# Kernel optimization log

Hardware: AMD Instinct MI355X
Metric: run time of the kernel (lower is better)

## Reference

```python
import jax, jax.numpy as jnp
import numpy as np

N, E, IN, H, O, K = 50000, 800000, 256, 128, 32, 5
ALPHA, EPS = 0.1, 1e-5


def setup_inputs() -> dict:
    key = jax.random.key(0)
    ks = jax.random.split(key, 20)
    nrm = lambda k, shape, s=0.02: jax.random.normal(k, shape, dtype=jnp.float32) * s
    H2 = H // 2
    return {
        "x": jax.random.normal(ks[0], (N, IN), dtype=jnp.float32),
        "edge_index": jax.random.randint(ks[1], (2, E), 0, N),
        "edge_weight": jax.random.uniform(ks[2], (E,), dtype=jnp.float32),
        # lin1 + bn1
        "W1": nrm(ks[3], (IN, H)), "b1": jnp.zeros((H,), jnp.float32),
        "g1": jnp.ones((H,), jnp.float32), "be1": jnp.zeros((H,), jnp.float32),
        "m1": nrm(ks[4], (H,), 0.1), "v1": 1.0 + 0.1 * jax.random.uniform(ks[5], (H,), dtype=jnp.float32),
        # lin2 + bn2
        "W2": nrm(ks[6], (H, H)), "b2": jnp.zeros((H,), jnp.float32),
        "g2": jnp.ones((H,), jnp.float32), "be2": jnp.zeros((H,), jnp.float32),
        "m2": nrm(ks[7], (H,), 0.1), "v2": 1.0 + 0.1 * jax.random.uniform(ks[8], (H,), dtype=jnp.float32),
        # attention over hop outputs (K+1)
        "att": jnp.ones((K + 1,), jnp.float32) + nrm(ks[9], (K + 1,), 0.1),
        # head: Linear(H, H//2) + BN + ReLU + Linear(H//2, O)
        "W3": nrm(ks[10], (H, H2)), "b3": jnp.zeros((H2,), jnp.float32),
        "g3": jnp.ones((H2,), jnp.float32), "be3": jnp.zeros((H2,), jnp.float32),
        "m3": nrm(ks[11], (H2,), 0.1), "v3": 1.0 + 0.1 * jax.random.uniform(ks[12], (H2,), dtype=jnp.float32),
        "W4": nrm(ks[13], (H2, O)), "b4": jnp.zeros((O,), jnp.float32),
    }


def _bn(t, g, b, m, v):
    # eval-mode BatchNorm1d using running stats
    return (t - m) * (g / jnp.sqrt(v + EPS)) + b


def reference(x, edge_index, edge_weight, W1, b1, g1, be1, m1, v1,
              W2, b2, g2, be2, m2, v2, att,
              W3, b3, g3, be3, m3, v3, W4, b4):
    n = x.shape[0]
    row, col = edge_index[0], edge_index[1]

    h = jax.nn.relu(_bn(x @ W1 + b1, g1, be1, m1, v1))
    identity = h
    h = jax.nn.relu(_bn(h @ W2 + b2, g2, be2, m2, v2)) + identity

    # weighted edge normalization: out-weight sum per source node, clamped >= 1
    wsum = jnp.maximum(jax.ops.segment_sum(edge_weight, row, num_segments=n), 1.0)
    edge_norm = edge_weight / wsum[row]  # [E]

    def prop(h_in):
        # APPNP-style: K inner iterations blending toward this call's h0
        h0 = h_in
        hk = h_in
        for _ in range(K):
            msg = hk[row] * edge_norm[:, None]          # [E, H] gather + scale
            agg = jax.ops.segment_sum(msg, col, num_segments=n)  # scatter-add
            hk = (1.0 - ALPHA) * agg + ALPHA * h0
        return hk

    xs = [h]
    hc = h
    for _ in range(K):  # outer loop: att has K+1 weights
        hc = prop(hc)
        xs.append(hc)

    stacked = jnp.stack(xs, axis=-1)          # [N, H, K+1]
    w = jax.nn.softmax(att)                   # [K+1]
    fused = jnp.einsum('nhk,k->nh', stacked, w)

    hid = jax.nn.relu(_bn(fused @ W3 + b3, g3, be3, m3, v3))
    return hid @ W4 + b4
```

## Files before the change

kernel.cpp:

```cpp
#include <hip/hip_runtime.h>
#include <cstddef>
#include <cstdint>

namespace {

constexpr int N   = 50000;
constexpr int E   = 800000;
constexpr int IN  = 256;
constexpr int H   = 128;
constexpr int H2v = 64;
constexpr int O   = 32;
constexpr int K   = 5;
constexpr float ALPHA = 0.1f;
constexpr float EPS   = 1e-5f;
constexpr int NPAD = 50048;
constexpr int CAP  = 48;
constexpr int NPW  = 4;
constexpr int PROP_BLOCKS = NPAD / (4 * NPW);
constexpr int NORM_BLOCKS = NPAD / 4;
constexpr int MLP_BLOCKS  = NPAD / 64;

typedef __bf16 bf16x8 __attribute__((ext_vector_type(8)));
typedef float  f32x4  __attribute__((ext_vector_type(4)));

__device__ inline uint32_t pack2_bf16(float x, float y) {
  uint32_t ux = __float_as_uint(x);
  uint32_t uy = __float_as_uint(y);
  ux = (ux + 0x7FFFu + ((ux >> 16) & 1u)) >> 16;
  uy = (uy + 0x7FFFu + ((uy >> 16) & 1u)) & 0xFFFF0000u;
  return uy | ux;
}
__device__ inline unsigned short bf16_1(float x) {
  uint32_t u = __float_as_uint(x);
  return (unsigned short)((u + 0x7FFFu + ((u >> 16) & 1u)) >> 16);
}
__device__ inline float bf16_lo(uint32_t v) { return __uint_as_float(v << 16); }
__device__ inline float bf16_hi(uint32_t v) { return __uint_as_float(v & 0xFFFF0000u); }
__device__ inline float bf16_f(unsigned short h) { return __uint_as_float(((uint32_t)h) << 16); }

__global__ void init_kernel(int* __restrict__ cnt, float* __restrict__ wsum,
                            const float* __restrict__ att, float* __restrict__ wk) {
  int i = blockIdx.x * blockDim.x + threadIdx.x;
  if (i < NPAD) cnt[i] = 0;
  if (i < N) wsum[i] = 0.f;
  if (i == 0) {
    float mx = att[0];
    for (int j = 1; j < K + 1; ++j) mx = fmaxf(mx, att[j]);
    float ex[K + 1];
    float s = 0.f;
    for (int j = 0; j < K + 1; ++j) { ex[j] = expf(att[j] - mx); s += ex[j]; }
    for (int j = 0; j < K + 1; ++j) wk[j] = ex[j] / s;
  }
}

__global__ void fused_fill_kernel(const int* __restrict__ row, const int* __restrict__ col,
                                  const float* __restrict__ ew,
                                  int* __restrict__ cnt, float* __restrict__ wsum,
                                  uint2* __restrict__ csr) {
  int i = blockIdx.x * blockDim.x + threadIdx.x;
  if (i < E) {
    int s = row[i];
    float w = ew[i];
    atomicAdd(&wsum[s], w);
    int d = col[i];
    int old = atomicAdd(&cnt[d], 1);
    if (old < CAP) csr[(size_t)d * CAP + old] = make_uint2((uint32_t)s, __float_as_uint(w));
  }
}

__global__ void conv_wt_kernel(const float* __restrict__ W, unsigned short* __restrict__ Wt,
                               int Kdim) {
  int t = blockIdx.x * blockDim.x + threadIdx.x;
  int k8 = Kdim / 8;
  int n = t / k8;
  int kk = (t % k8) * 8;
  if (n >= H) return;
  float f[8];
#pragma unroll
  for (int j = 0; j < 8; ++j) f[j] = W[(size_t)(kk + j) * H + n];
  uint4 pk;
  pk.x = pack2_bf16(f[0], f[1]);
  pk.y = pack2_bf16(f[2], f[3]);
  pk.z = pack2_bf16(f[4], f[5]);
  pk.w = pack2_bf16(f[6], f[7]);
  *(uint4*)&Wt[(size_t)n * Kdim + kk] = pk;
}

__global__ __launch_bounds__(256) void mlp1_mfma_kernel(
    const float* __restrict__ x, const unsigned short* __restrict__ Wt1,
    const float* __restrict__ b1, const float* __restrict__ g1,
    const float* __restrict__ be1, const float* __restrict__ m1,
    const float* __restrict__ v1, unsigned short* __restrict__ h1bf) {
  int wave = threadIdx.x >> 6;
  int lane = threadIdx.x & 63;
  int m_base = blockIdx.x * 64 + wave * 16;
  int idx16 = lane & 15;
  int quad = lane >> 4;
  int m = m_base + idx16;
  bf16x8 afrag[8];
  if (m < N) {
    const float* xrow = x + (size_t)m * IN + quad * 8;
#pragma unroll
    for (int k0 = 0; k0 < 8; ++k0) {
      float4 a = *(const float4*)(xrow + k0 * 32);
      float4 b = *(const float4*)(xrow + k0 * 32 + 4);
      uint4 pk;
      pk.x = pack2_bf16(a.x, a.y);
      pk.y = pack2_bf16(a.z, a.w);
      pk.z = pack2_bf16(b.x, b.y);
      pk.w = pack2_bf16(b.z, b.w);
      afrag[k0] = *(bf16x8*)&pk;
    }
  } else {
    uint4 z = {0, 0, 0, 0};
#pragma unroll
    for (int k0 = 0; k0 < 8; ++k0) afrag[k0] = *(bf16x8*)&z;
  }
#pragma unroll
  for (int n0 = 0; n0 < 8; ++n0) {
    f32x4 acc = {0.f, 0.f, 0.f, 0.f};
    const unsigned short* wrow = Wt1 + (size_t)(n0 * 16 + idx16) * IN + quad * 8;
#pragma unroll
    for (int k0 = 0; k0 < 8; ++k0) {
      bf16x8 bfrag = *(const bf16x8*)(wrow + k0 * 32);
      acc = __builtin_amdgcn_mfma_f32_16x16x32_bf16(afrag[k0], bfrag, acc, 0, 0, 0);
    }
    int n = n0 * 16 + idx16;
    float sc = g1[n] * rsqrtf(v1[n] + EPS);
    float ad = b1[n] - m1[n];
    float bb = be1[n];
#pragma unroll
    for (int r = 0; r < 4; ++r) {
      int mm = m_base + quad * 4 + r;
      float val = fmaxf((acc[r] + ad) * sc + bb, 0.f);
      h1bf[(size_t)mm * H + n] = bf16_1(val);
    }
  }
}

__device__ void norm_body(int bid, const int* __restrict__ cnt, const float* __restrict__ wsum,
                          uint2* __restrict__ csr) {
  int wave = threadIdx.x >> 6;
  int lane = threadIdx.x & 63;
  int node = bid * 4 + wave;
  if (node >= N) return;
  int deg = min(cnt[node], CAP);
  if (lane < deg) {
    size_t slot = (size_t)node * CAP + lane;
    uint2 e = csr[slot];
    float w = __uint_as_float(e.y) / fmaxf(wsum[e.x], 1.0f);
    csr[slot] = make_uint2(e.x, __float_as_uint(w));
  }
}

__device__ void mlp2_body(int bid, const unsigned short* __restrict__ h1bf,
                          const unsigned short* __restrict__ Wt2,
                          const float* __restrict__ b2, const float* __restrict__ g2,
                          const float* __restrict__ be2, const float* __restrict__ m2,
                          const float* __restrict__ v2, unsigned short* __restrict__ h0bf,
                          float* __restrict__ fused, const float* __restrict__ wk) {
  int wave = threadIdx.x >> 6;
  int lane = threadIdx.x & 63;
  int m_base = bid * 64 + wave * 16;
  int idx16 = lane & 15;
  int quad = lane >> 4;
  bf16x8 afrag[4];
  const unsigned short* arow = h1bf + (size_t)(m_base + idx16) * H + quad * 8;
#pragma unroll
  for (int k0 = 0; k0 < 4; ++k0) afrag[k0] = *(const bf16x8*)(arow + k0 * 32);
  float w0 = wk[0];
#pragma unroll
  for (int n0 = 0; n0 < 8; ++n0) {
    f32x4 acc = {0.f, 0.f, 0.f, 0.f};
    const unsigned short* wrow = Wt2 + (size_t)(n0 * 16 + idx16) * H + quad * 8;
#pragma unroll
    for (int k0 = 0; k0 < 4; ++k0) {
      bf16x8 bfrag = *(const bf16x8*)(wrow + k0 * 32);
      acc = __builtin_amdgcn_mfma_f32_16x16x32_bf16(afrag[k0], bfrag, acc, 0, 0, 0);
    }
    int n = n0 * 16 + idx16;
    float sc = g2[n] * rsqrtf(v2[n] + EPS);
    float ad = b2[n] - m2[n];
    float bb = be2[n];
#pragma unroll
    for (int r = 0; r < 4; ++r) {
      int m = m_base + quad * 4 + r;
      if (m < N) {
        float idv = bf16_f(h1bf[(size_t)m * H + n]);
        float val = fmaxf((acc[r] + ad) * sc + bb, 0.f) + idv;
        h0bf[(size_t)m * H + n] = bf16_1(val);
        fused[(size_t)m * H + n] = w0 * val;
      }
    }
  }
}

__global__ __launch_bounds__(256) void norm_mlp2_kernel(
    const int* __restrict__ cnt, const float* __restrict__ wsum,
    uint2* __restrict__ csr,
    const unsigned short* __restrict__ h1bf, const unsigned short* __restrict__ Wt2,
    const float* __restrict__ b2, const float* __restrict__ g2,
    const float* __restrict__ be2, const float* __restrict__ m2,
    const float* __restrict__ v2, unsigned short* __restrict__ h0bf,
    float* __restrict__ fused, const float* __restrict__ wk) {
  if ((int)blockIdx.x < NORM_BLOCKS)
    norm_body(blockIdx.x, cnt, wsum, csr);
  else
    mlp2_body(blockIdx.x - NORM_BLOCKS, h1bf, Wt2, b2, g2, be2, m2, v2, h0bf, fused, wk);
}

__global__ __launch_bounds__(256) void prop_kernel(
    const unsigned short* __restrict__ hk, const unsigned short* __restrict__ h0,
    unsigned short* __restrict__ outb,
    const int* __restrict__ cnt, const uint2* __restrict__ csr,
    float* __restrict__ fused, const float* __restrict__ wk, int wj) {
  int wave = threadIdx.x >> 6;
  int lane = threadIdx.x & 63;
  int quarter = lane >> 4;
  int colb = (lane & 15) * 8;
  int node0 = (blockIdx.x * 4 + wave) * NPW;
  float wj_w = (wj >= 0) ? wk[wj] : 0.f;
  for (int nn = 0; nn < NPW; ++nn) {
    int node = node0 + nn;
    int deg = min(cnt[node], CAP);
    int beg = node * CAP;
    int end = beg + deg;
    float a[8];
#pragma unroll
    for (int j = 0; j < 8; ++j) a[j] = 0.f;
    int nfull = deg >> 2;
    int qi = 0;
    for (; qi + 4 <= nfull; qi += 4) {
      uint2 ce[4];
      uint4 rv[4];
#pragma unroll
      for (int u = 0; u < 4; ++u) ce[u] = csr[beg + (qi + u) * 4 + quarter];
#pragma unroll
      for (int u = 0; u < 4; ++u) rv[u] = *(const uint4*)&hk[(size_t)ce[u].x * H + colb];
#pragma unroll
      for (int u = 0; u < 4; ++u) {
        float w = __uint_as_float(ce[u].y);
        a[0] += w * bf16_lo(rv[u].x); a[1] += w * bf16_hi(rv[u].x);
        a[2] += w * bf16_lo(rv[u].y); a[3] += w * bf16_hi(rv[u].y);
        a[4] += w * bf16_lo(rv[u].z); a[5] += w * bf16_hi(rv[u].z);
        a[6] += w * bf16_lo(rv[u].w); a[7] += w * bf16_hi(rv[u].w);
      }
    }
    for (; qi < nfull; ++qi) {
      uint2 ce = csr[beg + qi * 4 + quarter];
      uint4 rv = *(const uint4*)&hk[(size_t)ce.x * H + colb];
      float w = __uint_as_float(ce.y);
      a[0] += w * bf16_lo(rv.x); a[1] += w * bf16_hi(rv.x);
      a[2] += w * bf16_lo(rv.y); a[3] += w * bf16_hi(rv.y);
      a[4] += w * bf16_lo(rv.z); a[5] += w * bf16_hi(rv.z);
      a[6] += w * bf16_lo(rv.w); a[7] += w * bf16_hi(rv.w);
    }
    if (deg & 3) {
      int e = beg + nfull * 4 + quarter;
      bool valid = e < end;
      uint2 ce = csr[valid ? e : beg];
      float w = valid ? __uint_as_float(ce.y) : 0.f;
      uint4 rv = *(const uint4*)&hk[(size_t)ce.x * H + colb];
      a[0] += w * bf16_lo(rv.x); a[1] += w * bf16_hi(rv.x);
      a[2] += w * bf16_lo(rv.y); a[3] += w * bf16_hi(rv.y);
      a[4] += w * bf16_lo(rv.z); a[5] += w * bf16_hi(rv.z);
      a[6] += w * bf16_lo(rv.w); a[7] += w * bf16_hi(rv.w);
    }
#pragma unroll
    for (int j = 0; j < 8; ++j) {
      a[j] += __shfl_xor(a[j], 16, 64);
      a[j] += __shfl_xor(a[j], 32, 64);
    }
    size_t idx = (size_t)node * H + colb;
    if (quarter == 0) {
      uint4 hv = *(const uint4*)&h0[idx];
      float v0 = (1.f - ALPHA) * a[0] + ALPHA * bf16_lo(hv.x);
      float v1 = (1.f - ALPHA) * a[1] + ALPHA * bf16_hi(hv.x);
      float v2 = (1.f - ALPHA) * a[2] + ALPHA * bf16_lo(hv.y);
      float v3 = (1.f - ALPHA) * a[3] + ALPHA * bf16_hi(hv.y);
      float v4 = (1.f - ALPHA) * a[4] + ALPHA * bf16_lo(hv.z);
      float v5 = (1.f - ALPHA) * a[5] + ALPHA * bf16_hi(hv.z);
      float v6 = (1.f - ALPHA) * a[6] + ALPHA * bf16_lo(hv.w);
      float v7 = (1.f - ALPHA) * a[7] + ALPHA * bf16_hi(hv.w);
      uint4 pk;
      pk.x = pack2_bf16(v0, v1);
      pk.y = pack2_bf16(v2, v3);
      pk.z = pack2_bf16(v4, v5);
      pk.w = pack2_bf16(v6, v7);
      *(uint4*)&outb[idx] = pk;
    } else if (quarter == 1 && wj >= 0 && node < N) {
      uint4 hv = *(const uint4*)&h0[idx];
      float v0 = (1.f - ALPHA) * a[0] + ALPHA * bf16_lo(hv.x);
      float v1 = (1.f - ALPHA) * a[1] + ALPHA * bf16_hi(hv.x);
      float v2 = (1.f - ALPHA) * a[2] + ALPHA * bf16_lo(hv.y);
      float v3 = (1.f - ALPHA) * a[3] + ALPHA * bf16_hi(hv.y);
      float v4 = (1.f - ALPHA) * a[4] + ALPHA * bf16_lo(hv.z);
      float v5 = (1.f - ALPHA) * a[5] + ALPHA * bf16_hi(hv.z);
      float v6 = (1.f - ALPHA) * a[6] + ALPHA * bf16_lo(hv.w);
      float v7 = (1.f - ALPHA) * a[7] + ALPHA * bf16_hi(hv.w);
      float4 f0 = *(float4*)&fused[idx];
      float4 f1 = *(float4*)&fused[idx + 4];
      f0.x += wj_w * v0; f0.y += wj_w * v1; f0.z += wj_w * v2; f0.w += wj_w * v3;
      f1.x += wj_w * v4; f1.y += wj_w * v5; f1.z += wj_w * v6; f1.w += wj_w * v7;
      *(float4*)&fused[idx] = f0;
      *(float4*)&fused[idx + 4] = f1;
    }
  }
}

__global__ __launch_bounds__(64) void head_kernel(
    const float* __restrict__ fused, const float* __restrict__ W3,
    const float* __restrict__ b3, const float* __restrict__ g3,
    const float* __restrict__ be3, const float* __restrict__ m3,
    const float* __restrict__ v3, const float* __restrict__ W4,
    const float* __restrict__ b4, float* __restrict__ out) {
  __shared__ float fl[16][H];
  __shared__ float hl[16][H2v];
  int node0 = blockIdx.x * 16;
  int t = threadIdx.x;
  for (int idx = t * 4; idx < 16 * H; idx += 64 * 4) {
    int r = idx >> 7, c = idx & (H - 1);
    *(float4*)&fl[r][c] = *(const float4*)&fused[(size_t)(node0 + r) * H + c];
  }
  __syncthreads();
  {
    int ng = t >> 4;
    int c0 = (t & 15) * 4;
    float acc[4][4];
#pragma unroll
    for (int a = 0; a < 4; ++a)
#pragma unroll
      for (int b = 0; b < 4; ++b) acc[a][b] = 0.f;
    for (int k = 0; k < H; k += 4) {
      float4 xv[4];
#pragma unroll
      for (int a = 0; a < 4; ++a) xv[a] = *(const float4*)&fl[ng * 4 + a][k];
      float4 wv[4];
#pragma unroll
      for (int j = 0; j < 4; ++j) wv[j] = *(const float4*)&W3[(size_t)(k + j) * H2v + c0];
#pragma unroll
      for (int a = 0; a < 4; ++a) {
        float xa0 = xv[a].x, xa1 = xv[a].y, xa2 = xv[a].z, xa3 = xv[a].w;
        acc[a][0] += xa0 * wv[0].x + xa1 * wv[1].x + xa2 * wv[2].x + xa3 * wv[3].x;
        acc[a][1] += xa0 * wv[0].y + xa1 * wv[1].y + xa2 * wv[2].y + xa3 * wv[3].y;
        acc[a][2] += xa0 * wv[0].z + xa1 * wv[1].z + xa2 * wv[2].z + xa3 * wv[3].z;
        acc[a][3] += xa0 * wv[0].w + xa1 * wv[1].w + xa2 * wv[2].w + xa3 * wv[3].w;
      }
    }
    float sc[4], ad[4], bb[4];
#pragma unroll
    for (int b = 0; b < 4; ++b) {
      int c = c0 + b;
      sc[b] = g3[c] * rsqrtf(v3[c] + EPS);
      ad[b] = b3[c] - m3[c];
      bb[b] = be3[c];
    }
#pragma unroll
    for (int a = 0; a < 4; ++a)
#pragma unroll
      for (int b = 0; b < 4; ++b)
        hl[ng * 4 + a][c0 + b] = fmaxf((acc[a][b] + ad[b]) * sc[b] + bb[b], 0.f);
  }
  __syncthreads();
  {
    int co = t & 31;
    int nh = t >> 5;
    float bias = b4[co];
#pragma unroll
    for (int a = 0; a < 8; ++a) {
      int nloc = nh * 8 + a;
      float accf = bias;
      for (int k = 0; k < H2v; k += 4) {
        float4 hv = *(const float4*)&hl[nloc][k];
        accf += hv.x * W4[(size_t)(k + 0) * O + co];
        accf += hv.y * W4[(size_t)(k + 1) * O + co];
        accf += hv.z * W4[(size_t)(k + 2) * O + co];
        accf += hv.w * W4[(size_t)(k + 3) * O + co];
      }
      out[(size_t)(node0 + nloc) * O + co] = accf;
    }
  }
}

}

extern "C" void kernel_launch(void* const* d_in, const int* in_sizes, int n_in,
                              void* d_out, int out_size, void* d_ws, size_t ws_size,
                              hipStream_t stream) {
  const float* x   = (const float*)d_in[0];
  const int*   ei  = (const int*)d_in[1];
  const float* ew  = (const float*)d_in[2];
  const float* W1  = (const float*)d_in[3];
  const float* b1  = (const float*)d_in[4];
  const float* g1  = (const float*)d_in[5];
  const float* be1 = (const float*)d_in[6];
  const float* m1  = (const float*)d_in[7];
  const float* v1  = (const float*)d_in[8];
  const float* W2  = (const float*)d_in[9];
  const float* b2  = (const float*)d_in[10];
  const float* g2  = (const float*)d_in[11];
  const float* be2 = (const float*)d_in[12];
  const float* m2  = (const float*)d_in[13];
  const float* v2  = (const float*)d_in[14];
  const float* att = (const float*)d_in[15];
  const float* W3  = (const float*)d_in[16];
  const float* b3  = (const float*)d_in[17];
  const float* g3  = (const float*)d_in[18];
  const float* be3 = (const float*)d_in[19];
  const float* m3  = (const float*)d_in[20];
  const float* v3  = (const float*)d_in[21];
  const float* W4  = (const float*)d_in[22];
  const float* b4  = (const float*)d_in[23];
  const int* row = ei;
  const int* col = ei + E;
  float* out = (float*)d_out;

  char* p = (char*)d_ws;
  auto carve = [&](size_t bytes) -> void* {
    void* q = (void*)p;
    p += (bytes + 255) & ~(size_t)255;
    return q;
  };
  int*      cnt  = (int*)carve((size_t)NPAD * 4);
  float*    wsum = (float*)carve((size_t)N * 4);
  uint2*    csr  = (uint2*)carve((size_t)N * CAP * 8);
  float*    wk   = (float*)carve(64);
  unsigned short* Wt1  = (unsigned short*)carve((size_t)H * IN * 2);
  unsigned short* Wt2  = (unsigned short*)carve((size_t)H * H * 2);
  unsigned short* h1bf = (unsigned short*)carve((size_t)NPAD * H * 2);
  unsigned short* bf0  = (unsigned short*)carve((size_t)NPAD * H * 2);
  unsigned short* bfA  = (unsigned short*)carve((size_t)NPAD * H * 2);
  unsigned short* bfB  = (unsigned short*)carve((size_t)NPAD * H * 2);
  float* fused = (float*)carve((size_t)N * H * 4);

  const int tb = 256;
  init_kernel<<<(NPAD + tb - 1) / tb, tb, 0, stream>>>(cnt, wsum, att, wk);
  conv_wt_kernel<<<(H * (IN / 8) + tb - 1) / tb, tb, 0, stream>>>(W1, Wt1, IN);
  conv_wt_kernel<<<(H * (H / 8) + tb - 1) / tb, tb, 0, stream>>>(W2, Wt2, H);

  fused_fill_kernel<<<(E + tb - 1) / tb, tb, 0, stream>>>(row, col, ew, cnt, wsum, csr);
  mlp1_mfma_kernel<<<MLP_BLOCKS, 256, 0, stream>>>(x, Wt1, b1, g1, be1, m1, v1, h1bf);
  norm_mlp2_kernel<<<NORM_BLOCKS + MLP_BLOCKS, 256, 0, stream>>>(
      cnt, wsum, csr, h1bf, Wt2, b2, g2, be2, m2, v2, bf0, fused, wk);

  unsigned short* h0 = bf0;
  unsigned short* pa = bfA;
  unsigned short* pb = bfB;
  for (int j = 1; j <= K; ++j) {
    const unsigned short* src = h0;
    unsigned short* dst = pa;
    for (int i = 0; i < K; ++i) {
      int wj = (i == K - 1) ? j : -1;
      prop_kernel<<<PROP_BLOCKS, 256, 0, stream>>>(src, h0, dst, cnt, csr, fused, wk, wj);
      if (i < K - 1) {
        src = dst;
        dst = (dst == pa) ? pb : pa;
      }
    }
    unsigned short* oldh0 = h0;
    h0 = pa;
    pa = pb;
    pb = oldh0;
  }

  head_kernel<<<N / 16, 64, 0, stream>>>(fused, W3, b3, g3, be3, m3, v3, W4, b4, out);
}
```

Before: 1.222 ms.

## Slice propagation features into 16-column panels and pack CSR entries to 32 bits

Node features for propagation are now stored as 8 column slices of 16 bf16 values each, laid out as [slice][node][16]. Propagation blocks are split by slice, so each block's random gathers stay inside a roughly 1.6MB working set that can stay cache-resident. The CSR entries shrink from 8 to 4 bytes: a 16-bit source index plus a bf16 edge weight, which cuts edge-list traffic. The trade-offs are gathers of only 8 bytes per lane, eight times more blocks that each re-read the CSR, lower precision on edge weights, and a hard dependence on N staying below 65536.

```diff
diff --git a/kernel.cpp b/kernel.cpp
--- a/kernel.cpp
+++ b/kernel.cpp
@@ -15,8 +15,8 @@
 constexpr float EPS   = 1e-5f;
 constexpr int NPAD = 50048;
 constexpr int CAP  = 48;
-constexpr int NPW  = 4;
-constexpr int PROP_BLOCKS = NPAD / (4 * NPW);
+constexpr int NPW  = 8;
+constexpr int PROP_BLOCKS = 8 * (NPAD / (4 * NPW));
 constexpr int NORM_BLOCKS = NPAD / 4;
 constexpr int MLP_BLOCKS  = NPAD / 64;
 
@@ -56,7 +56,7 @@
 __global__ void fused_fill_kernel(const int* __restrict__ row, const int* __restrict__ col,
                                   const float* __restrict__ ew,
                                   int* __restrict__ cnt, float* __restrict__ wsum,
-                                  uint2* __restrict__ csr) {
+                                  uint32_t* __restrict__ csr4) {
   int i = blockIdx.x * blockDim.x + threadIdx.x;
   if (i < E) {
     int s = row[i];
@@ -64,7 +64,8 @@
     atomicAdd(&wsum[s], w);
     int d = col[i];
     int old = atomicAdd(&cnt[d], 1);
-    if (old < CAP) csr[(size_t)d * CAP + old] = make_uint2((uint32_t)s, __float_as_uint(w));
+    if (old < CAP)
+      csr4[(size_t)d * CAP + old] = (uint32_t)s | ((uint32_t)bf16_1(w) << 16);
   }
 }
 
@@ -139,7 +140,7 @@
 }
 
 __device__ void norm_body(int bid, const int* __restrict__ cnt, const float* __restrict__ wsum,
-                          uint2* __restrict__ csr) {
+                          uint32_t* __restrict__ csr4) {
   int wave = threadIdx.x >> 6;
   int lane = threadIdx.x & 63;
   int node = bid * 4 + wave;
@@ -147,9 +148,10 @@
   int deg = min(cnt[node], CAP);
   if (lane < deg) {
     size_t slot = (size_t)node * CAP + lane;
-    uint2 e = csr[slot];
-    float w = __uint_as_float(e.y) / fmaxf(wsum[e.x], 1.0f);
-    csr[slot] = make_uint2(e.x, __float_as_uint(w));
+    uint32_t cw = csr4[slot];
+    uint32_t src = cw & 0xFFFFu;
+    float w = bf16_hi(cw) / fmaxf(wsum[src], 1.0f);
+    csr4[slot] = src | ((uint32_t)bf16_1(w) << 16);
   }
 }
 
@@ -188,7 +190,7 @@
       if (m < N) {
         float idv = bf16_f(h1bf[(size_t)m * H + n]);
         float val = fmaxf((acc[r] + ad) * sc + bb, 0.f) + idv;
-        h0bf[(size_t)m * H + n] = bf16_1(val);
+        h0bf[((size_t)n0 * NPAD + m) * 16 + idx16] = bf16_1(val);
         fused[(size_t)m * H + n] = w0 * val;
       }
     }
@@ -197,14 +199,14 @@
 
 __global__ __launch_bounds__(256) void norm_mlp2_kernel(
     const int* __restrict__ cnt, const float* __restrict__ wsum,
-    uint2* __restrict__ csr,
+    uint32_t* __restrict__ csr4,
     const unsigned short* __restrict__ h1bf, const unsigned short* __restrict__ Wt2,
     const float* __restrict__ b2, const float* __restrict__ g2,
     const float* __restrict__ be2, const float* __restrict__ m2,
     const float* __restrict__ v2, unsigned short* __restrict__ h0bf,
     float* __restrict__ fused, const float* __restrict__ wk) {
   if ((int)blockIdx.x < NORM_BLOCKS)
-    norm_body(blockIdx.x, cnt, wsum, csr);
+    norm_body(blockIdx.x, cnt, wsum, csr4);
   else
     mlp2_body(blockIdx.x - NORM_BLOCKS, h1bf, Wt2, b2, g2, be2, m2, v2, h0bf, fused, wk);
 }
@@ -212,98 +214,66 @@
 __global__ __launch_bounds__(256) void prop_kernel(
     const unsigned short* __restrict__ hk, const unsigned short* __restrict__ h0,
     unsigned short* __restrict__ outb,
-    const int* __restrict__ cnt, const uint2* __restrict__ csr,
+    const int* __restrict__ cnt, const uint32_t* __restrict__ csr4,
     float* __restrict__ fused, const float* __restrict__ wk, int wj) {
   int wave = threadIdx.x >> 6;
   int lane = threadIdx.x & 63;
-  int quarter = lane >> 4;
-  int colb = (lane & 15) * 8;
-  int node0 = (blockIdx.x * 4 + wave) * NPW;
+  int grp  = blockIdx.x & 7;
+  int nodeblk = blockIdx.x >> 3;
+  int node0 = (nodeblk * 4 + wave) * NPW;
+  int epos = lane >> 2;
+  int cpos = lane & 3;
+  size_t slice = (size_t)grp * NPAD * 16;
   float wj_w = (wj >= 0) ? wk[wj] : 0.f;
   for (int nn = 0; nn < NPW; ++nn) {
     int node = node0 + nn;
     int deg = min(cnt[node], CAP);
     int beg = node * CAP;
-    int end = beg + deg;
-    float a[8];
-#pragma unroll
-    for (int j = 0; j < 8; ++j) a[j] = 0.f;
-    int nfull = deg >> 2;
-    int qi = 0;
-    for (; qi + 4 <= nfull; qi += 4) {
-      uint2 ce[4];
-      uint4 rv[4];
-#pragma unroll
-      for (int u = 0; u < 4; ++u) ce[u] = csr[beg + (qi + u) * 4 + quarter];
-#pragma unroll
-      for (int u = 0; u < 4; ++u) rv[u] = *(const uint4*)&hk[(size_t)ce[u].x * H + colb];
-#pragma unroll
-      for (int u = 0; u < 4; ++u) {
-        float w = __uint_as_float(ce[u].y);
-        a[0] += w * bf16_lo(rv[u].x); a[1] += w * bf16_hi(rv[u].x);
-        a[2] += w * bf16_lo(rv[u].y); a[3] += w * bf16_hi(rv[u].y);
-        a[4] += w * bf16_lo(rv[u].z); a[5] += w * bf16_hi(rv[u].z);
-        a[6] += w * bf16_lo(rv[u].w); a[7] += w * bf16_hi(rv[u].w);
-      }
-    }
-    for (; qi < nfull; ++qi) {
-      uint2 ce = csr[beg + qi * 4 + quarter];
-      uint4 rv = *(const uint4*)&hk[(size_t)ce.x * H + colb];
-      float w = __uint_as_float(ce.y);
-      a[0] += w * bf16_lo(rv.x); a[1] += w * bf16_hi(rv.x);
-      a[2] += w * bf16_lo(rv.y); a[3] += w * bf16_hi(rv.y);
-      a[4] += w * bf16_lo(rv.z); a[5] += w * bf16_hi(rv.z);
-      a[6] += w * bf16_lo(rv.w); a[7] += w * bf16_hi(rv.w);
-    }
-    if (deg & 3) {
-      int e = beg + nfull * 4 + quarter;
-      bool valid = e < end;
-      uint2 ce = csr[valid ? e : beg];
-      float w = valid ? __uint_as_float(ce.y) : 0.f;
-      uint4 rv = *(const uint4*)&hk[(size_t)ce.x * H + colb];
-      a[0] += w * bf16_lo(rv.x); a[1] += w * bf16_hi(rv.x);
-      a[2] += w * bf16_lo(rv.y); a[3] += w * bf16_hi(rv.y);
-      a[4] += w * bf16_lo(rv.z); a[5] += w * bf16_hi(rv.z);
-      a[6] += w * bf16_lo(rv.w); a[7] += w * bf16_hi(rv.w);
-    }
-#pragma unroll
-    for (int j = 0; j < 8; ++j) {
-      a[j] += __shfl_xor(a[j], 16, 64);
-      a[j] += __shfl_xor(a[j], 32, 64);
-    }
-    size_t idx = (size_t)node * H + colb;
-    if (quarter == 0) {
-      uint4 hv = *(const uint4*)&h0[idx];
-      float v0 = (1.f - ALPHA) * a[0] + ALPHA * bf16_lo(hv.x);
-      float v1 = (1.f - ALPHA) * a[1] + ALPHA * bf16_hi(hv.x);
-      float v2 = (1.f - ALPHA) * a[2] + ALPHA * bf16_lo(hv.y);
-      float v3 = (1.f - ALPHA) * a[3] + ALPHA * bf16_hi(hv.y);
-      float v4 = (1.f - ALPHA) * a[4] + ALPHA * bf16_lo(hv.z);
-      float v5 = (1.f - ALPHA) * a[5] + ALPHA * bf16_hi(hv.z);
-      float v6 = (1.f - ALPHA) * a[6] + ALPHA * bf16_lo(hv.w);
-      float v7 = (1.f - ALPHA) * a[7] + ALPHA * bf16_hi(hv.w);
-      uint4 pk;
+    float a0 = 0.f, a1 = 0.f, a2 = 0.f, a3 = 0.f;
+    int ngr = (deg + 15) >> 4;
+    for (int gi = 0; gi < ngr; ++gi) {
+      int e = gi * 16 + epos;
+      bool v = e < deg;
+      uint32_t cw = csr4[beg + (v ? e : 0)];
+      float w = v ? bf16_hi(cw) : 0.f;
+      uint32_t src = cw & 0xFFFFu;
+      uint2 rv = *(const uint2*)&hk[slice + (size_t)src * 16 + cpos * 4];
+      a0 += w * bf16_lo(rv.x);
+      a1 += w * bf16_hi(rv.x);
+      a2 += w * bf16_lo(rv.y);
+      a3 += w * bf16_hi(rv.y);
+    }
+#pragma unroll
+    for (int d = 4; d < 64; d <<= 1) {
+      a0 += __shfl_xor(a0, d, 64);
+      a1 += __shfl_xor(a1, d, 64);
+      a2 += __shfl_xor(a2, d, 64);
+      a3 += __shfl_xor(a3, d, 64);
+    }
+    size_t sidx = slice + (size_t)node * 16 + cpos * 4;
+    if (epos == 0) {
+      uint2 hv = *(const uint2*)&h0[sidx];
+      float v0 = (1.f - ALPHA) * a0 + ALPHA * bf16_lo(hv.x);
+      float v1 = (1.f - ALPHA) * a1 + ALPHA * bf16_hi(hv.x);
+      float v2 = (1.f - ALPHA) * a2 + ALPHA * bf16_lo(hv.y);
+      float v3 = (1.f - ALPHA) * a3 + ALPHA * bf16_hi(hv.y);
+      uint2 pk;
       pk.x = pack2_bf16(v0, v1);
       pk.y = pack2_bf16(v2, v3);
-      pk.z = pack2_bf16(v4, v5);
-      pk.w = pack2_bf16(v6, v7);
-      *(uint4*)&outb[idx] = pk;
-    } else if (quarter == 1 && wj >= 0 && node < N) {
-      uint4 hv = *(const uint4*)&h0[idx];
-      float v0 = (1.f - ALPHA) * a[0] + ALPHA * bf16_lo(hv.x);
-      float v1 = (1.f - ALPHA) * a[1] + ALPHA * bf16_hi(hv.x);
-      float v2 = (1.f - ALPHA) * a[2] + ALPHA * bf16_lo(hv.y);
-      float v3 = (1.f - ALPHA) * a[3] + ALPHA * bf16_hi(hv.y);
-      float v4 = (1.f - ALPHA) * a[4] + ALPHA * bf16_lo(hv.z);
-      float v5 = (1.f - ALPHA) * a[5] + ALPHA * bf16_hi(hv.z);
-      float v6 = (1.f - ALPHA) * a[6] + ALPHA * bf16_lo(hv.w);
-      float v7 = (1.f - ALPHA) * a[7] + ALPHA * bf16_hi(hv.w);
-      float4 f0 = *(float4*)&fused[idx];
-      float4 f1 = *(float4*)&fused[idx + 4];
-      f0.x += wj_w * v0; f0.y += wj_w * v1; f0.z += wj_w * v2; f0.w += wj_w * v3;
-      f1.x += wj_w * v4; f1.y += wj_w * v5; f1.z += wj_w * v6; f1.w += wj_w * v7;
-      *(float4*)&fused[idx] = f0;
-      *(float4*)&fused[idx + 4] = f1;
+      *(uint2*)&outb[sidx] = pk;
+    } else if (epos == 1 && wj >= 0 && node < N) {
+      uint2 hv = *(const uint2*)&h0[sidx];
+      float v0 = (1.f - ALPHA) * a0 + ALPHA * bf16_lo(hv.x);
+      float v1 = (1.f - ALPHA) * a1 + ALPHA * bf16_hi(hv.x);
+      float v2 = (1.f - ALPHA) * a2 + ALPHA * bf16_lo(hv.y);
+      float v3 = (1.f - ALPHA) * a3 + ALPHA * bf16_hi(hv.y);
+      size_t fidx = (size_t)node * H + grp * 16 + cpos * 4;
+      float4 f = *(float4*)&fused[fidx];
+      f.x += wj_w * v0;
+      f.y += wj_w * v1;
+      f.z += wj_w * v2;
+      f.w += wj_w * v3;
+      *(float4*)&fused[fidx] = f;
     }
   }
 }
@@ -423,7 +393,7 @@
   };
   int*      cnt  = (int*)carve((size_t)NPAD * 4);
   float*    wsum = (float*)carve((size_t)N * 4);
-  uint2*    csr  = (uint2*)carve((size_t)N * CAP * 8);
+  uint32_t* csr4 = (uint32_t*)carve((size_t)N * CAP * 4);
   float*    wk   = (float*)carve(64);
   unsigned short* Wt1  = (unsigned short*)carve((size_t)H * IN * 2);
   unsigned short* Wt2  = (unsigned short*)carve((size_t)H * H * 2);
@@ -438,10 +408,10 @@
   conv_wt_kernel<<<(H * (IN / 8) + tb - 1) / tb, tb, 0, stream>>>(W1, Wt1, IN);
   conv_wt_kernel<<<(H * (H / 8) + tb - 1) / tb, tb, 0, stream>>>(W2, Wt2, H);
 
-  fused_fill_kernel<<<(E + tb - 1) / tb, tb, 0, stream>>>(row, col, ew, cnt, wsum, csr);
+  fused_fill_kernel<<<(E + tb - 1) / tb, tb, 0, stream>>>(row, col, ew, cnt, wsum, csr4);
   mlp1_mfma_kernel<<<MLP_BLOCKS, 256, 0, stream>>>(x, Wt1, b1, g1, be1, m1, v1, h1bf);
   norm_mlp2_kernel<<<NORM_BLOCKS + MLP_BLOCKS, 256, 0, stream>>>(
-      cnt, wsum, csr, h1bf, Wt2, b2, g2, be2, m2, v2, bf0, fused, wk);
+      cnt, wsum, csr4, h1bf, Wt2, b2, g2, be2, m2, v2, bf0, fused, wk);
 
   unsigned short* h0 = bf0;
   unsigned short* pa = bfA;
@@ -451,7 +421,7 @@
     unsigned short* dst = pa;
     for (int i = 0; i < K; ++i) {
       int wj = (i == K - 1) ? j : -1;
-      prop_kernel<<<PROP_BLOCKS, 256, 0, stream>>>(src, h0, dst, cnt, csr, fused, wk, wj);
+      prop_kernel<<<PROP_BLOCKS, 256, 0, stream>>>(src, h0, dst, cnt, csr4, fused, wk, wj);
       if (i < K - 1) {
         src = dst;
         dst = (dst == pa) ? pb : pa;
```

Result: slower. 2.947 ms (+141.1%).
